# Performance work log

Hardware: AMD Instinct MI355X
Metric: run time of the kernel (lower is better)

The kernel has to match this reference:

```python
import jax, jax.numpy as jnp
import numpy as np

RADIUS = 0.07          # gno_config.gno_radius
SCALES = (1.0, 2.0)    # gno_config.scales


def _kernel_mlp(pair, kW1, kb1, kW2, kb2, kW3, kb3):
    # ChannelMLP inside IntegralTransform: gelu between layers, none after last
    h = jax.nn.gelu(pair @ kW1 + kb1)
    h = jax.nn.gelu(h @ kW2 + kb2)
    return h @ kW3 + kb3


def setup_inputs() -> dict:
    key = jax.random.key(0)
    ks = jax.random.split(key, 8)
    B, N, NL, CD, IN_C, C, H = 2, 2048, 512, 2, 16, 32, 32

    def glorot(k, shape):
        return jax.random.normal(k, shape) / jnp.sqrt(jnp.float32(shape[0]))

    return {
        "x_coord": jax.random.uniform(ks[0], (B, N, CD), dtype=jnp.float32),
        "pndata": jax.random.normal(ks[1], (B, N, IN_C), dtype=jnp.float32),
        "latent_tokens_coord": jax.random.uniform(ks[2], (NL, CD), dtype=jnp.float32),
        # lifting ChannelMLP (n_layers=1 -> single 1x1 conv == linear)
        "W_lift": glorot(ks[3], (IN_C, C)),
        "b_lift": jnp.zeros((C,), jnp.float32),
        # kernel MLP: [2*coord_dim=4] -> 32 -> 32 -> out_channels=32
        "kW1": glorot(ks[4], (2 * CD, H)),
        "kb1": jnp.zeros((H,), jnp.float32),
        "kW2": glorot(ks[5], (H, H)),
        "kb2": jnp.zeros((H,), jnp.float32),
        "kW3": glorot(ks[6], (H, C)),
        "kb3": jnp.zeros((C,), jnp.float32),
    }


def reference(x_coord, pndata, latent_tokens_coord,
              W_lift, b_lift, kW1, kb1, kW2, kb2, kW3, kb3):
    # lifting: [B,N,in_c] -> [B,N,C]
    f = pndata @ W_lift + b_lift

    B, N, CD = x_coord.shape
    NL = latent_tokens_coord.shape[0]

    y = x_coord[:, None, :, :]                      # [B,1,N,CD] source coords
    xq = latent_tokens_coord[None, :, None, :]      # [1,NL,1,CD] query coords
    # kernel input = cat(y_j, x_i) per (query i, source j) pair -> [B,NL,N,2*CD]
    pair = jnp.concatenate([jnp.broadcast_to(y, (B, NL, N, CD)),
                            jnp.broadcast_to(xq, (B, NL, N, CD))], axis=-1)
    kvals = _kernel_mlp(pair, kW1, kb1, kW2, kb2, kW3, kb3)  # [B,NL,N,C]

    d2 = jnp.sum((y - xq) ** 2, axis=-1)            # [B,NL,N] squared distances

    out = jnp.zeros((B, NL, kvals.shape[-1]), f.dtype)
    for s in SCALES:  # fixed small set of scales (2)
        # radius neighbor search expressed as dense mask (faithful to ball query)
        mask = (d2 <= (RADIUS * s) ** 2).astype(f.dtype)      # [B,NL,N]
        cnt = jnp.maximum(jnp.sum(mask, axis=-1), 1.0)        # [B,NL]
        # 'linear' transform: mean_j k(x_i,y_j) * f(y_j) over neighbors
        agg = jnp.einsum('bijc,bjc,bij->bic', kvals, f, mask)
        out = out + agg / cnt[..., None]
    return out  # [B,NL,C]
```

## Files before the change

kernel.cpp:

```cpp
#include <hip/hip_runtime.h>

static constexpr int B_ = 2, N_ = 2048, NL_ = 512, IN_C_ = 16, C_ = 32, H_ = 32;
static constexpr float R1SQ = (float)(0.07 * 0.07);
static constexpr float R2SQ = (float)(0.14 * 0.14);

typedef __attribute__((ext_vector_type(8))) short bf16x8;
typedef __attribute__((ext_vector_type(4))) float f32x4;

__device__ __forceinline__ float gelu_tanh(float x) {
    float z2 = 2.0f * 0.7978845608028654f * x * fmaf(0.044715f * x, x, 1.0f);
    float e = __expf(z2);
    return x * (1.0f - 1.0f / (e + 1.0f));
}

__device__ __forceinline__ short f2bf(float x) {
    unsigned u = __float_as_uint(x);
    u += 0x7fffu + ((u >> 16) & 1u);
    return (short)(u >> 16);
}

__global__ __launch_bounds__(256)
void lift_kernel(const float* __restrict__ pnd,
                 const float* __restrict__ Wl, const float* __restrict__ bl,
                 float* __restrict__ f)
{
    __shared__ float sW[IN_C_ * C_];
    __shared__ float sb[C_];
    int tid = threadIdx.x;
    for (int idx = tid; idx < IN_C_ * C_; idx += 256) sW[idx] = Wl[idx];
    if (tid < C_) sb[tid] = bl[tid];
    __syncthreads();
    int c = tid & 31;
    int row = blockIdx.x * 8 + (tid >> 5);
    if (row >= B_ * N_) return;
    const float* p = pnd + (size_t)row * IN_C_;
    float s = sb[c];
#pragma unroll
    for (int m = 0; m < IN_C_; ++m) s = fmaf(p[m], sW[m * C_ + c], s);
    f[(size_t)row * C_ + c] = s;
}

__global__ __launch_bounds__(256)
void magno_mfma(const float* __restrict__ x_coord,
                const float* __restrict__ lat,
                const float* __restrict__ kW1, const float* __restrict__ kb1,
                const float* __restrict__ kW2, const float* __restrict__ kb2,
                const float* __restrict__ kW3, const float* __restrict__ kb3,
                const float* __restrict__ f,
                float* __restrict__ out)
{
    __shared__ float sR0[H_], sR1[H_], sA1[H_];
    __shared__ unsigned jlist[N_];
    __shared__ __align__(16) short strans[4][64 * 40];
    __shared__ float sred[4][C_];
    __shared__ int s_n, s_c1;

    const int tid  = threadIdx.x;
    const int lane = tid & 63;
    const int wid  = tid >> 6;
    const int qd   = lane >> 4;
    const int li   = lane & 15;
    const int bi = blockIdx.x;
    const int b = bi >> 9, i = bi & (NL_ - 1);
    const float xq0 = lat[2 * i], xq1 = lat[2 * i + 1];

    bf16x8 w2f[2], w3f[2];
#pragma unroll
    for (int nt = 0; nt < 2; ++nt) {
        int n0 = li + 16 * nt;
#pragma unroll
        for (int jj = 0; jj < 8; ++jj) {
            int k = qd * 8 + jj;
            w2f[nt][jj] = f2bf(kW2[k * H_ + n0]);
            w3f[nt][jj] = f2bf(kW3[k * C_ + n0]);
        }
    }
    const float b2A = kb2[li], b2B = kb2[li + 16];
    const float b3A = kb3[li], b3B = kb3[li + 16];

    if (tid == 0) { s_n = 0; s_c1 = 0; }
    if (tid < H_) {
        sR0[tid] = kW1[tid];
        sR1[tid] = kW1[H_ + tid];
        sA1[tid] = fmaf(xq0, kW1[2 * H_ + tid], fmaf(xq1, kW1[3 * H_ + tid], kb1[tid]));
    }
    __syncthreads();

    const float2* __restrict__ xc = (const float2*)(x_coord + (size_t)b * N_ * 2);
    const unsigned long long ltmask = (1ull << lane) - 1ull;
    float2 ys[8];
#pragma unroll
    for (int t = 0; t < 8; ++t) ys[t] = xc[tid + 256 * t];
#pragma unroll
    for (int t = 0; t < 8; ++t) {
        float dy0 = ys[t].x - xq0, dy1 = ys[t].y - xq1;
        float d2 = dy0 * dy0 + dy1 * dy1;
        bool in2 = d2 <= R2SQ;
        bool in1 = d2 <= R1SQ;
        unsigned long long m2 = __ballot(in2);
        unsigned long long m1 = __ballot(in1);
        int basew = 0;
        if (lane == 0) {
            basew = atomicAdd(&s_n, __popcll(m2));
            atomicAdd(&s_c1, __popcll(m1));
        }
        basew = __shfl(basew, 0, 64);
        if (in2) {
            int pos = basew + __popcll(m2 & ltmask);
            jlist[pos] = (unsigned)(tid + 256 * t) | (in1 ? 0x80000000u : 0u);
        }
    }
    __syncthreads();
    const int n = s_n;
    const float inv2 = 1.0f / (float)(n > 0 ? n : 1);
    const float inv1 = 1.0f / (float)(s_c1 > 0 ? s_c1 : 1);

    float r0v[8], r1v[8], a1v[8];
#pragma unroll
    for (int jj = 0; jj < 8; ++jj) {
        int k = qd * 8 + jj;
        r0v[jj] = sR0[k]; r1v[jj] = sR1[k]; a1v[jj] = sA1[k];
    }

    short* tb = &strans[wid][0];
    const float* __restrict__ fbase = f + (size_t)b * N_ * C_;

    float accA = 0.0f, accB = 0.0f;
    const int nIter = (n + 255) >> 8;

    for (int it = 0; it < nIter; ++it) {
        const int base = it * 256 + 64 * wid;
        const bool active = (base < n);

        bf16x8 h2f[4];
        f32x4 accF_unused;
        f32x4 acc2[4][2];
        if (active) {
            bf16x8 hfrag[4];
#pragma unroll
            for (int mt = 0; mt < 4; ++mt) {
                int e = base + 16 * mt + li;
                unsigned pk = jlist[e < N_ ? e : 0];
                int j = (int)(pk & (unsigned)(N_ - 1));
                float2 y = xc[j];
#pragma unroll
                for (int jj = 0; jj < 8; ++jj)
                    hfrag[mt][jj] = f2bf(gelu_tanh(fmaf(y.x, r0v[jj], fmaf(y.y, r1v[jj], a1v[jj]))));
            }
#pragma unroll
            for (int mt = 0; mt < 4; ++mt)
#pragma unroll
                for (int nt = 0; nt < 2; ++nt) {
                    f32x4 z = {0.f, 0.f, 0.f, 0.f};
                    acc2[mt][nt] = __builtin_amdgcn_mfma_f32_16x16x32_bf16(hfrag[mt], w2f[nt], z, 0, 0, 0);
                }
#pragma unroll
            for (int mt = 0; mt < 4; ++mt)
#pragma unroll
                for (int nt = 0; nt < 2; ++nt) {
                    float bb = nt ? b2B : b2A;
                    int hid = li + 16 * nt;
#pragma unroll
                    for (int r = 0; r < 4; ++r) {
                        int entry = 16 * mt + 4 * qd + r;
                        tb[entry * 40 + hid] = f2bf(gelu_tanh(acc2[mt][nt][r] + bb));
                    }
                }
        }
        __syncthreads();
        if (active) {
#pragma unroll
            for (int mt = 0; mt < 4; ++mt)
                h2f[mt] = *(const bf16x8*)&tb[(li + 16 * mt) * 40 + qd * 8];
        }
        __syncthreads();
        if (active) {
            f32x4 acc3[4][2];
#pragma unroll
            for (int mt = 0; mt < 4; ++mt)
#pragma unroll
                for (int nt = 0; nt < 2; ++nt) {
                    f32x4 z = {0.f, 0.f, 0.f, 0.f};
                    acc3[mt][nt] = __builtin_amdgcn_mfma_f32_16x16x32_bf16(h2f[mt], w3f[nt], z, 0, 0, 0);
                }
#pragma unroll
            for (int mt = 0; mt < 4; ++mt)
#pragma unroll
                for (int r = 0; r < 4; ++r) {
                    int e = base + 16 * mt + 4 * qd + r;
                    unsigned pk = jlist[e < N_ ? e : 0];
                    int j = (int)(pk & (unsigned)(N_ - 1));
                    float w = (e < n) ? (inv2 + ((pk & 0x80000000u) ? inv1 : 0.0f)) : 0.0f;
                    const float* fr = fbase + (size_t)j * C_;
                    float fA = fr[li], fB = fr[li + 16];
                    accA = fmaf(w * fA, acc3[mt][0][r] + b3A, accA);
                    accB = fmaf(w * fB, acc3[mt][1][r] + b3B, accB);
                }
        }
    }

    accA += __shfl_xor(accA, 16, 64);
    accA += __shfl_xor(accA, 32, 64);
    accB += __shfl_xor(accB, 16, 64);
    accB += __shfl_xor(accB, 32, 64);
    if (lane < 16) {
        sred[wid][li] = accA;
        sred[wid][li + 16] = accB;
    }
    __syncthreads();
    if (tid < C_)
        out[(size_t)bi * C_ + tid] = (sred[0][tid] + sred[1][tid]) + (sred[2][tid] + sred[3][tid]);
}

extern "C" void kernel_launch(void* const* d_in, const int* in_sizes, int n_in,
                              void* d_out, int out_size, void* d_ws, size_t ws_size,
                              hipStream_t stream) {
    const float* x_coord = (const float*)d_in[0];
    const float* pndata  = (const float*)d_in[1];
    const float* lat     = (const float*)d_in[2];
    const float* W_lift  = (const float*)d_in[3];
    const float* b_lift  = (const float*)d_in[4];
    const float* kW1     = (const float*)d_in[5];
    const float* kb1     = (const float*)d_in[6];
    const float* kW2     = (const float*)d_in[7];
    const float* kb2     = (const float*)d_in[8];
    const float* kW3     = (const float*)d_in[9];
    const float* kb3     = (const float*)d_in[10];
    float* out = (float*)d_out;

    float* f = (float*)d_ws;
    lift_kernel<<<(B_ * N_ + 7) / 8, 256, 0, stream>>>(pndata, W_lift, b_lift, f);
    magno_mfma<<<B_ * NL_, 256, 0, stream>>>(
        x_coord, lat, kW1, kb1, kW2, kb2, kW3, kb3, f, out);
}
```

Baseline: 95.12 us.

## Give each wave its own neighbor list and prefetch f rows early

Neighbor compaction now builds a per-wave list over a contiguous 512-point chunk, with no shared atomics, and the loop count uses the largest wave's count. The f-row gathers are hoisted ahead of the MLP compute so their latency overlaps the MFMA work. W2/W3 are staged through LDS, and the GELU uses a hardware reciprocal. The aim is less atomic contention and hidden gather latency, at the cost of load imbalance across waves and more registers held live.

```diff
diff --git a/kernel.cpp b/kernel.cpp
--- a/kernel.cpp
+++ b/kernel.cpp
@@ -10,7 +10,8 @@
 __device__ __forceinline__ float gelu_tanh(float x) {
     float z2 = 2.0f * 0.7978845608028654f * x * fmaf(0.044715f * x, x, 1.0f);
     float e = __expf(z2);
-    return x * (1.0f - 1.0f / (e + 1.0f));
+    float t = __builtin_amdgcn_rcpf(e + 1.0f);
+    return x - x * t;
 }
 
 __device__ __forceinline__ short f2bf(float x) {
@@ -49,11 +50,12 @@
                 const float* __restrict__ f,
                 float* __restrict__ out)
 {
+    __shared__ float sW23[2][H_ * H_];
     __shared__ float sR0[H_], sR1[H_], sA1[H_];
-    __shared__ unsigned jlist[N_];
+    __shared__ unsigned jlist[4][512];
     __shared__ __align__(16) short strans[4][64 * 40];
     __shared__ float sred[4][C_];
-    __shared__ int s_n, s_c1;
+    __shared__ int scnt[4][2];
 
     const int tid  = threadIdx.x;
     const int lane = tid & 63;
@@ -64,33 +66,24 @@
     const int b = bi >> 9, i = bi & (NL_ - 1);
     const float xq0 = lat[2 * i], xq1 = lat[2 * i + 1];
 
-    bf16x8 w2f[2], w3f[2];
-#pragma unroll
-    for (int nt = 0; nt < 2; ++nt) {
-        int n0 = li + 16 * nt;
-#pragma unroll
-        for (int jj = 0; jj < 8; ++jj) {
-            int k = qd * 8 + jj;
-            w2f[nt][jj] = f2bf(kW2[k * H_ + n0]);
-            w3f[nt][jj] = f2bf(kW3[k * C_ + n0]);
-        }
-    }
-    const float b2A = kb2[li], b2B = kb2[li + 16];
-    const float b3A = kb3[li], b3B = kb3[li + 16];
-
-    if (tid == 0) { s_n = 0; s_c1 = 0; }
+    for (int idx = tid; idx < H_ * H_; idx += 256) {
+        sW23[0][idx] = kW2[idx];
+        sW23[1][idx] = kW3[idx];
+    }
     if (tid < H_) {
         sR0[tid] = kW1[tid];
         sR1[tid] = kW1[H_ + tid];
         sA1[tid] = fmaf(xq0, kW1[2 * H_ + tid], fmaf(xq1, kW1[3 * H_ + tid], kb1[tid]));
     }
-    __syncthreads();
+    const float b2A = kb2[li], b2B = kb2[li + 16];
+    const float b3A = kb3[li], b3B = kb3[li + 16];
 
     const float2* __restrict__ xc = (const float2*)(x_coord + (size_t)b * N_ * 2);
     const unsigned long long ltmask = (1ull << lane) - 1ull;
     float2 ys[8];
 #pragma unroll
-    for (int t = 0; t < 8; ++t) ys[t] = xc[tid + 256 * t];
+    for (int t = 0; t < 8; ++t) ys[t] = xc[512 * wid + 64 * t + lane];
+    int cnt = 0, c1w = 0;
 #pragma unroll
     for (int t = 0; t < 8; ++t) {
         float dy0 = ys[t].x - xq0, dy1 = ys[t].y - xq1;
@@ -99,21 +92,37 @@
         bool in1 = d2 <= R1SQ;
         unsigned long long m2 = __ballot(in2);
         unsigned long long m1 = __ballot(in1);
-        int basew = 0;
-        if (lane == 0) {
-            basew = atomicAdd(&s_n, __popcll(m2));
-            atomicAdd(&s_c1, __popcll(m1));
-        }
-        basew = __shfl(basew, 0, 64);
         if (in2) {
-            int pos = basew + __popcll(m2 & ltmask);
-            jlist[pos] = (unsigned)(tid + 256 * t) | (in1 ? 0x80000000u : 0u);
-        }
-    }
+            int pos = cnt + __popcll(m2 & ltmask);
+            jlist[wid][pos] = (unsigned)(512 * wid + 64 * t + lane) | (in1 ? 0x80000000u : 0u);
+        }
+        cnt += __popcll(m2);
+        c1w += __popcll(m1);
+    }
+    if (lane == 0) { scnt[wid][0] = cnt; scnt[wid][1] = c1w; }
     __syncthreads();
-    const int n = s_n;
-    const float inv2 = 1.0f / (float)(n > 0 ? n : 1);
-    const float inv1 = 1.0f / (float)(s_c1 > 0 ? s_c1 : 1);
+
+    const int n   = scnt[0][0] + scnt[1][0] + scnt[2][0] + scnt[3][0];
+    const int c1  = scnt[0][1] + scnt[1][1] + scnt[2][1] + scnt[3][1];
+    int nmax = scnt[0][0];
+    nmax = scnt[1][0] > nmax ? scnt[1][0] : nmax;
+    nmax = scnt[2][0] > nmax ? scnt[2][0] : nmax;
+    nmax = scnt[3][0] > nmax ? scnt[3][0] : nmax;
+    const float inv2 = 1.0f / (float)(n  > 0 ? n  : 1);
+    const float inv1 = 1.0f / (float)(c1 > 0 ? c1 : 1);
+    const int nIter = (nmax + 63) >> 6;
+
+    bf16x8 w2f[2], w3f[2];
+#pragma unroll
+    for (int nt = 0; nt < 2; ++nt) {
+        int n0 = li + 16 * nt;
+#pragma unroll
+        for (int jj = 0; jj < 8; ++jj) {
+            int k = qd * 8 + jj;
+            w2f[nt][jj] = f2bf(sW23[0][k * H_ + n0]);
+            w3f[nt][jj] = f2bf(sW23[1][k * H_ + n0]);
+        }
+    }
 
     float r0v[8], r1v[8], a1v[8];
 #pragma unroll
@@ -123,30 +132,43 @@
     }
 
     short* tb = &strans[wid][0];
+    const unsigned* __restrict__ jl = &jlist[wid][0];
     const float* __restrict__ fbase = f + (size_t)b * N_ * C_;
 
     float accA = 0.0f, accB = 0.0f;
-    const int nIter = (n + 255) >> 8;
 
     for (int it = 0; it < nIter; ++it) {
-        const int base = it * 256 + 64 * wid;
-        const bool active = (base < n);
+        const int base = it * 64;
+        const bool active = (base < cnt);
 
         bf16x8 h2f[4];
-        f32x4 accF_unused;
-        f32x4 acc2[4][2];
+        float fAv[4][4], fBv[4][4];
         if (active) {
+#pragma unroll
+            for (int mt = 0; mt < 4; ++mt)
+#pragma unroll
+                for (int r = 0; r < 4; ++r) {
+                    int el = base + 16 * mt + 4 * qd + r;
+                    unsigned pk = jl[el & 511];
+                    int j = (int)(pk & (unsigned)(N_ - 1));
+                    const float* fr = fbase + (size_t)j * C_;
+                    fAv[mt][r] = fr[li];
+                    fBv[mt][r] = fr[li + 16];
+                }
+
             bf16x8 hfrag[4];
 #pragma unroll
             for (int mt = 0; mt < 4; ++mt) {
                 int e = base + 16 * mt + li;
-                unsigned pk = jlist[e < N_ ? e : 0];
+                unsigned pk = jl[e & 511];
                 int j = (int)(pk & (unsigned)(N_ - 1));
                 float2 y = xc[j];
 #pragma unroll
                 for (int jj = 0; jj < 8; ++jj)
                     hfrag[mt][jj] = f2bf(gelu_tanh(fmaf(y.x, r0v[jj], fmaf(y.y, r1v[jj], a1v[jj]))));
             }
+
+            f32x4 acc2[4][2];
 #pragma unroll
             for (int mt = 0; mt < 4; ++mt)
 #pragma unroll
@@ -154,6 +176,7 @@
                     f32x4 z = {0.f, 0.f, 0.f, 0.f};
                     acc2[mt][nt] = __builtin_amdgcn_mfma_f32_16x16x32_bf16(hfrag[mt], w2f[nt], z, 0, 0, 0);
                 }
+
 #pragma unroll
             for (int mt = 0; mt < 4; ++mt)
 #pragma unroll
@@ -187,14 +210,11 @@
             for (int mt = 0; mt < 4; ++mt)
 #pragma unroll
                 for (int r = 0; r < 4; ++r) {
-                    int e = base + 16 * mt + 4 * qd + r;
-                    unsigned pk = jlist[e < N_ ? e : 0];
-                    int j = (int)(pk & (unsigned)(N_ - 1));
-                    float w = (e < n) ? (inv2 + ((pk & 0x80000000u) ? inv1 : 0.0f)) : 0.0f;
-                    const float* fr = fbase + (size_t)j * C_;
-                    float fA = fr[li], fB = fr[li + 16];
-                    accA = fmaf(w * fA, acc3[mt][0][r] + b3A, accA);
-                    accB = fmaf(w * fB, acc3[mt][1][r] + b3B, accB);
+                    int el = base + 16 * mt + 4 * qd + r;
+                    unsigned pk = jl[el & 511];
+                    float w = (el < cnt) ? (inv2 + ((pk & 0x80000000u) ? inv1 : 0.0f)) : 0.0f;
+                    accA = fmaf(w * fAv[mt][r], acc3[mt][0][r] + b3A, accA);
+                    accB = fmaf(w * fBv[mt][r], acc3[mt][1][r] + b3B, accB);
                 }
         }
     }
```

New measurement: 92.23 us. -3.0%, faster.
